# Kernel optimization log

Measured on AMD Instinct MI355X. Metric: run time of the kernel, lower is better.

## Reference

```python
import jax, jax.numpy as jnp
import numpy as np

B = 256        # trees per batch
DEPTH = 10     # complete binary tree depth -> 2^10 - 1 = 1023 internal nodes
N = 2**DEPTH - 1
IN = 128       # input_size
H = 128        # hidden_size
C = 5          # num_classes


def setup_inputs() -> dict:
    key = jax.random.key(0)
    ks = jax.random.split(key, 13)
    gdim = IN + 2 * H  # concat(x, h_left, h_right)
    inp = {"x": jax.random.normal(ks[0], (B, N, IN), jnp.float32)}
    names = ["i", "fl", "fr", "o", "u"]
    for j, nm in enumerate(names):
        inp[f"W_{nm}"] = 0.05 * jax.random.normal(ks[1 + 2 * j], (H, gdim), jnp.float32)
        inp[f"b_{nm}"] = 0.05 * jax.random.normal(ks[2 + 2 * j], (H,), jnp.float32)
    inp["W_cls"] = 0.05 * jax.random.normal(ks[11], (C, H), jnp.float32)
    inp["b_cls"] = 0.05 * jax.random.normal(ks[12], (C,), jnp.float32)
    return inp


def reference(x, W_i, b_i, W_fl, b_fl, W_fr, b_fr, W_o, b_o, W_u, b_u, W_cls, b_cls):
    # Level-order complete binary tree: node k has children 2k+1, 2k+2.
    # Bottom-up sweep; below the deepest internal level all children are
    # empty nodes with h = c = 0 (matches the original base case).
    Bb = x.shape[0]
    h = jnp.zeros((Bb, 2 ** DEPTH, H), x.dtype)
    c = jnp.zeros_like(h)
    for d in range(DEPTH - 1, -1, -1):  # fixed, small structural loop
        n = 2 ** d
        start = n - 1  # level-order offset of level d
        xs = x[:, start:start + n]            # [B, n, IN]
        hl, hr = h[:, 0::2], h[:, 1::2]       # children of node j are 2j, 2j+1 (level-local)
        cl, cr = c[:, 0::2], c[:, 1::2]
        comb = jnp.concatenate([xs, hl, hr], axis=-1)  # [B, n, IN+2H]
        lin = lambda W, b: jnp.einsum('bng,og->bno', comb, W) + b
        i = jax.nn.sigmoid(lin(W_i, b_i))
        fl = jax.nn.sigmoid(lin(W_fl, b_fl))
        fr = jax.nn.sigmoid(lin(W_fr, b_fr))
        o = jax.nn.sigmoid(lin(W_o, b_o))
        u = jnp.tanh(lin(W_u, b_u))
        c = i * u + fl * cl + fr * cr
        h = o * jnp.tanh(c)
    root_h = h[:, 0]                          # [B, H]
    logits = root_h @ W_cls.T + b_cls         # [B, C]
    return logits
```

## Files before the change

kernel.cpp:

```cpp
#include <hip/hip_runtime.h>
#include <hip/hip_bf16.h>
#include <stdint.h>


#define BATCH 256
#define NTOT 1023
#define HDIM 128
#define NCLS 5
#define GDIM 384

typedef __bf16 bf16x8 __attribute__((ext_vector_type(8)));
typedef float f32x4 __attribute__((ext_vector_type(4)));

__device__ __forceinline__ float sigmoid_f(float v) { return 1.f / (1.f + __expf(-v)); }
__device__ __forceinline__ float tanh_f(float v) { return 1.f - 2.f / (1.f + __expf(2.f * v)); }

__device__ __forceinline__ void load_lds16(const void* g, void* l) {
  __builtin_amdgcn_global_load_lds((const __attribute__((address_space(1))) unsigned int*)g,
                                   (__attribute__((address_space(3))) unsigned int*)l, 16, 0, 0);
}

__global__ __launch_bounds__(256) void pack_w(
    const float* __restrict__ W0, const float* __restrict__ W1, const float* __restrict__ W2,
    const float* __restrict__ W3, const float* __restrict__ W4, __bf16* __restrict__ PW)
{
  int t = blockIdx.x * 256 + threadIdx.x;
  int lane = t & 63;
  int chunk = t >> 6;
  int ks = chunk % 12;
  int jf = (chunk / 12) & 7;
  int g = chunk / 96;
  const float* W = (g == 0) ? W0 : (g == 1) ? W1 : (g == 2) ? W2 : (g == 3) ? W3 : W4;
  const float* s = W + (size_t)(jf * 16 + (lane & 15)) * GDIM + ks * 32 + (lane >> 4) * 8;
  float4 v0 = *(const float4*)s;
  float4 v1 = *(const float4*)(s + 4);
  bf16x8 w;
  w[0] = (__bf16)v0.x; w[1] = (__bf16)v0.y; w[2] = (__bf16)v0.z; w[3] = (__bf16)v0.w;
  w[4] = (__bf16)v1.x; w[5] = (__bf16)v1.y; w[6] = (__bf16)v1.z; w[7] = (__bf16)v1.w;
  *(bf16x8*)(PW + (size_t)t * 8) = w;
}

__constant__ int GM_LEAF[3] = {0, 3, 4};

template<bool LEAF>
__device__ __forceinline__ void tile_body(
    const float* __restrict__ x, const __bf16* __restrict__ PW,
    const __bf16* __restrict__ h_prev, const float* __restrict__ c_prev,
    __bf16* __restrict__ h_out, float* __restrict__ c_out,
    const float* __restrict__ bv0, const float* __restrict__ bv1,
    const float* __restrict__ bv2, const float* __restrict__ bv3,
    const float* __restrict__ bv4,
    int d, int m0, int j0, unsigned char* lds)
{
  const int tid = threadIdx.x;
  const int w = tid >> 6;
  const int l = tid & 63;
  const int l15 = l & 15;
  const int quad = l >> 4;
  const int q8 = quad * 8;
  const int n = 1 << d;
  const int jfb = j0 >> 4;
  constexpr int NACC = LEAF ? 3 : 5;
  constexpr int NCH = 4 * NACC;
  constexpr int BUFS = NCH * 1024;
  constexpr int NKT = LEAF ? 4 : 12;
  constexpr int NQ = NCH / 4;

  const int ms = m0 + w * 16 + l15;
  const int bs = ms >> d;
  const int ids = ms & (n - 1);
  const float* xr = x + ((size_t)bs * NTOT + (n - 1) + ids) * HDIM + q8;
  const __bf16* hr = LEAF ? (const __bf16*)nullptr
                          : h_prev + ((size_t)bs * 2 * n + 2 * ids) * HDIM + q8;

  auto stageB = [&](int t, int wks) {
    unsigned char* Bb = lds + (t & 1) * BUFS;
#pragma unroll
    for (int q = 0; q < NQ; ++q) {
      int c = w + q * 4;
      int ai = c >> 2, jfl = c & 3;
      int g = LEAF ? GM_LEAF[ai] : ai;
      const __bf16* src = PW + (((size_t)(g * 8 + jfb + jfl) * 12 + wks) * 64 + l) * 8;
      load_lds16(src, Bb + c * 1024);
    }
  };

  stageB(0, LEAF ? 0 : 4);

  bf16x8 xf[4];
#pragma unroll
  for (int kx = 0; kx < 4; ++kx) {
    float4 v0 = *(const float4*)(xr + kx * 32);
    float4 v1 = *(const float4*)(xr + kx * 32 + 4);
    bf16x8 t;
    t[0] = (__bf16)v0.x; t[1] = (__bf16)v0.y; t[2] = (__bf16)v0.z; t[3] = (__bf16)v0.w;
    t[4] = (__bf16)v1.x; t[5] = (__bf16)v1.y; t[6] = (__bf16)v1.z; t[7] = (__bf16)v1.w;
    xf[kx] = t;
  }

  bf16x8 ah[2];
  if constexpr (!LEAF) ah[0] = *(const bf16x8*)(hr);

  f32x4 acc[4][NACC];
#pragma unroll
  for (int jfl = 0; jfl < 4; ++jfl)
#pragma unroll
    for (int ai = 0; ai < NACC; ++ai)
      acc[jfl][ai] = (f32x4){0.f, 0.f, 0.f, 0.f};

#pragma unroll
  for (int t = 0; t < NKT; ++t) {
    __syncthreads();
    if (t + 1 < NKT) {
      stageB(t + 1, LEAF ? (t + 1) : ((t + 5) % 12));
      if constexpr (!LEAF) {
        if (t + 1 < 8) {
          const int o = ((t + 1) < 4) ? 0 : 1;
          ah[(t + 1) & 1] = *(const bf16x8*)(hr + o * HDIM + ((t + 1) & 3) * 32);
        }
      }
    }
    bf16x8 a;
    if constexpr (LEAF) a = xf[t];
    else a = (t < 8) ? ah[t & 1] : xf[t - 8];
    const unsigned char* Bb = lds + (t & 1) * BUFS;
#pragma unroll
    for (int ai = 0; ai < NACC; ++ai) {
#pragma unroll
      for (int jfl = 0; jfl < 4; ++jfl) {
        bf16x8 bb = *(const bf16x8*)(Bb + (ai * 4 + jfl) * 1024 + l * 16);
        acc[jfl][ai] = __builtin_amdgcn_mfma_f32_16x16x32_bf16(a, bb, acc[jfl][ai], 0, 0, 0);
      }
    }
  }

#pragma unroll
  for (int jfl = 0; jfl < 4; ++jfl) {
    const int je = j0 + jfl * 16 + l15;
    const float b0 = bv0[je], b3 = bv3[je], b4 = bv4[je];
#pragma unroll
    for (int r = 0; r < 4; ++r) {
      const int me = m0 + w * 16 + quad * 4 + r;
      const int b = me >> d;
      const int id = me & (n - 1);
      float gi = sigmoid_f(acc[jfl][0][r] + b0);
      float go = sigmoid_f(acc[jfl][LEAF ? 1 : 3][r] + b3);
      float gu = tanh_f(acc[jfl][LEAF ? 2 : 4][r] + b4);
      float cv = gi * gu;
      if constexpr (!LEAF) {
        float gl = sigmoid_f(acc[jfl][1][r] + bv1[je]);
        float gr = sigmoid_f(acc[jfl][2][r] + bv2[je]);
        size_t cbase = ((size_t)b * 2 * n + 2 * id) * HDIM + je;
        cv += gl * c_prev[cbase] + gr * c_prev[cbase + HDIM];
      }
      size_t ob = ((size_t)b * n + id) * HDIM + je;
      c_out[ob] = cv;
      h_out[ob] = (__bf16)(go * tanh_f(cv));
    }
  }
}

template<bool LEAF>
__global__ __launch_bounds__(256, (LEAF ? 5 : 4)) void level_kernel(
    const float* __restrict__ x, const __bf16* __restrict__ PW,
    const float* __restrict__ bv0, const float* __restrict__ bv1,
    const float* __restrict__ bv2, const float* __restrict__ bv3,
    const float* __restrict__ bv4,
    const __bf16* __restrict__ h_prev, const float* __restrict__ c_prev,
    __bf16* __restrict__ h_out, float* __restrict__ c_out, int d)
{
  __shared__ unsigned char lds[LEAF ? 24576 : 40960];
  tile_body<LEAF>(x, PW, h_prev, c_prev, h_out, c_out,
                  bv0, bv1, bv2, bv3, bv4, d,
                  (int)blockIdx.x * 64, (int)blockIdx.y * 64, lds);
}

#define TB_P  81920
#define TB_Q  132096
#define CSTR  132

__global__ __launch_bounds__(256, 1) void tail_kernel(
    const float* __restrict__ x, const __bf16* __restrict__ PW,
    const float* __restrict__ bv0, const float* __restrict__ bv1,
    const float* __restrict__ bv2, const float* __restrict__ bv3,
    const float* __restrict__ bv4,
    const float* __restrict__ Wcls, const float* __restrict__ bcls,
    const __bf16* __restrict__ h6, const float* __restrict__ c6,
    float* __restrict__ out)
{
  __shared__ unsigned char lds[157184];
  const int b = blockIdx.x;
  const int tid = threadIdx.x;
  const int w = tid >> 6;
  const int l = tid & 63;
  const int l15 = l & 15;
  const int quad = l >> 4;
  const int q8 = quad * 8;

  unsigned char* Ph = lds + TB_P;
  float* Pc = (float*)(lds + TB_P + 16384);
  unsigned char* Qh = lds + TB_Q;
  float* Qc = (float*)(lds + TB_Q + 8192);

  {
    const __bf16* hs = h6 + (size_t)b * 64 * HDIM;
#pragma unroll
    for (int it = 0; it < 4; ++it) {
      int idx = it * 256 + tid;
      int node = idx >> 4, i8 = idx & 15;
      bf16x8 v = *(const bf16x8*)(hs + node * HDIM + i8 * 8);
      *(bf16x8*)(Ph + node * 256 + ((i8 * 16) ^ ((node & 7) << 4))) = v;
    }
    const float* cs = c6 + (size_t)b * 64 * HDIM;
#pragma unroll
    for (int it = 0; it < 8; ++it) {
      int idx = it * 256 + tid;
      int node = idx >> 5, seg = idx & 31;
      float4 v = *(const float4*)(cs + node * HDIM + seg * 4);
      *(float4*)(Pc + node * CSTR + seg * 4) = v;
    }
  }

  for (int d = 5; d >= 0; --d) {
    const int s = 5 - d;
    const int n = 1 << d;
    const int nmf = (d == 5) ? 2 : 1;
    unsigned char* prev_h = (s & 1) ? Qh : Ph;
    float*         prev_c = (s & 1) ? Qc : Pc;
    unsigned char* cur_h  = (s & 1) ? Ph : Qh;
    float*         cur_c  = (s & 1) ? Pc : Qc;

    bf16x8 xf[2][4];
#pragma unroll
    for (int mf = 0; mf < 2; ++mf) {
      const float* xr = x + ((size_t)b * NTOT + (n - 1) + mf * 16 + l15) * HDIM + q8;
#pragma unroll
      for (int ks = 0; ks < 4; ++ks) {
        float4 v0 = *(const float4*)(xr + ks * 32);
        float4 v1 = *(const float4*)(xr + ks * 32 + 4);
        bf16x8 t;
        t[0] = (__bf16)v0.x; t[1] = (__bf16)v0.y; t[2] = (__bf16)v0.z; t[3] = (__bf16)v0.w;
        t[4] = (__bf16)v1.x; t[5] = (__bf16)v1.y; t[6] = (__bf16)v1.z; t[7] = (__bf16)v1.w;
        xf[mf][ks] = t;
      }
    }

    auto stageB = [&](int ks) {
      unsigned char* Bb = lds + (ks & 1) * 40960;
#pragma unroll
      for (int q = 0; q < 10; ++q) {
        int c = w * 10 + q;
        const __bf16* src = PW + ((size_t)(c * 12 + ks) * 64 + l) * 8;
        load_lds16(src, Bb + c * 1024);
      }
    };

    f32x4 acc[2][2][5];
#pragma unroll
    for (int mf = 0; mf < 2; ++mf)
#pragma unroll
      for (int jfl = 0; jfl < 2; ++jfl)
#pragma unroll
        for (int g = 0; g < 5; ++g)
          acc[mf][jfl][g] = (f32x4){0.f, 0.f, 0.f, 0.f};

    stageB(0);
    for (int ks = 0; ks < 12; ++ks) {
      __syncthreads();
      if (ks < 11) stageB(ks + 1);
      const unsigned char* Bb = lds + (ks & 1) * 40960;
      bf16x8 a0, a1;
      if (ks < 4) {
        a0 = xf[0][ks];
        a1 = xf[1][ks];
      } else {
        const int o = (ks < 8) ? 0 : 1;
        const int col2 = (((ks - (o ? 8 : 4)) * 32) + q8) * 2;
        int n0 = 2 * l15 + o;
        int n1 = 2 * (16 + l15) + o;
        a0 = *(const bf16x8*)(prev_h + n0 * 256 + (col2 ^ ((n0 & 7) << 4)));
        a1 = *(const bf16x8*)(prev_h + n1 * 256 + (col2 ^ ((n1 & 7) << 4)));
      }
#pragma unroll
      for (int g = 0; g < 5; ++g) {
#pragma unroll
        for (int jfl = 0; jfl < 2; ++jfl) {
          bf16x8 bb = *(const bf16x8*)(Bb + (g * 8 + w * 2 + jfl) * 1024 + l * 16);
          acc[0][jfl][g] = __builtin_amdgcn_mfma_f32_16x16x32_bf16(a0, bb, acc[0][jfl][g], 0, 0, 0);
          if (nmf == 2)
            acc[1][jfl][g] = __builtin_amdgcn_mfma_f32_16x16x32_bf16(a1, bb, acc[1][jfl][g], 0, 0, 0);
        }
      }
    }

#pragma unroll
    for (int jfl = 0; jfl < 2; ++jfl) {
      const int je = w * 32 + jfl * 16 + l15;
      const float b0 = bv0[je], b1 = bv1[je], b2 = bv2[je], b3 = bv3[je], b4 = bv4[je];
#pragma unroll
      for (int mf = 0; mf < 2; ++mf) {
#pragma unroll
        for (int r = 0; r < 4; ++r) {
          const int me = mf * 16 + quad * 4 + r;
          if (me < n) {
            float gi = sigmoid_f(acc[mf][jfl][0][r] + b0);
            float gl = sigmoid_f(acc[mf][jfl][1][r] + b1);
            float gr = sigmoid_f(acc[mf][jfl][2][r] + b2);
            float go = sigmoid_f(acc[mf][jfl][3][r] + b3);
            float gu = tanh_f(acc[mf][jfl][4][r] + b4);
            float cv = gi * gu + gl * prev_c[(2 * me) * CSTR + je]
                               + gr * prev_c[(2 * me + 1) * CSTR + je];
            cur_c[me * CSTR + je] = cv;
            *(__bf16*)(cur_h + me * 256 + ((je * 2) ^ ((me & 7) << 4))) =
                (__bf16)(go * tanh_f(cv));
          }
        }
      }
    }
  }

  __syncthreads();
  if (tid < NCLS) {
    float sacc = bcls[tid];
    for (int k = 0; k < HDIM; ++k)
      sacc += (float)(*(const __bf16*)(Ph + k * 2)) * Wcls[tid * HDIM + k];
    out[(size_t)b * NCLS + tid] = sacc;
  }
}

extern "C" void kernel_launch(void* const* d_in, const int* in_sizes, int n_in,
                              void* d_out, int out_size, void* d_ws, size_t ws_size,
                              hipStream_t stream) {
  const float* x  = (const float*)d_in[0];
  const float* W[5]  = {(const float*)d_in[1], (const float*)d_in[3], (const float*)d_in[5],
                        (const float*)d_in[7], (const float*)d_in[9]};
  const float* bv[5] = {(const float*)d_in[2], (const float*)d_in[4], (const float*)d_in[6],
                        (const float*)d_in[8], (const float*)d_in[10]};
  const float* Wcls = (const float*)d_in[11];
  const float* bcls = (const float*)d_in[12];

  uint8_t* ws = (uint8_t*)d_ws;
  __bf16* hb0 = (__bf16*)ws;
  __bf16* hb1 = (__bf16*)(ws + 33554432);
  float*  cb0 = (float*)(ws + 50331648);
  float*  cb1 = (float*)(ws + 117440512);
  __bf16* PW  = (__bf16*)(ws + 150994944);

  pack_w<<<120, 256, 0, stream>>>(W[0], W[1], W[2], W[3], W[4], PW);

  level_kernel<true><<<dim3(2048, 2), 256, 0, stream>>>(
      x, PW, bv[0], bv[1], bv[2], bv[3], bv[4], hb1, cb1, hb0, cb0, 9);
  for (int d = 8; d >= 6; --d) {
    const int p = 9 - d;
    __bf16* h_out = (p & 1) ? hb1 : hb0;
    float*  c_out = (p & 1) ? cb1 : cb0;
    const __bf16* h_prev = (p & 1) ? hb0 : hb1;
    const float*  c_prev = (p & 1) ? cb0 : cb1;
    dim3 grid((BATCH << d) >> 6, 2);
    level_kernel<false><<<grid, 256, 0, stream>>>(
        x, PW, bv[0], bv[1], bv[2], bv[3], bv[4], h_prev, c_prev, h_out, c_out, d);
  }
  tail_kernel<<<BATCH, 256, 0, stream>>>(
      x, PW, bv[0], bv[1], bv[2], bv[3], bv[4],
      Wcls, bcls, hb1, cb1, (float*)d_out);
}
```

Before: 499.7 us.

## Fuse levels 9 through 6 into one subtree kernel keeping h/c in LDS

Replaces the four per-level kernel launches for depths 9..6 with a single kernel where each 512-thread block processes a 64-leaf subtree of one tree through four levels. Intermediate h (bf16, XOR-swizzled) and c stay in LDS, so they no longer round-trip through global memory between levels, and each block now computes all 128 hidden columns against the full weight set. In exchange there is one block per CU with 157 KB of LDS, shrinking M-tiles at upper levels (down to 8 valid rows), and weights re-streamed per block.

```diff
diff --git a/kernel.cpp b/kernel.cpp
--- a/kernel.cpp
+++ b/kernel.cpp
@@ -40,17 +40,22 @@
   *(bf16x8*)(PW + (size_t)t * 8) = w;
 }
 
-__constant__ int GM_LEAF[3] = {0, 3, 4};
-
-template<bool LEAF>
-__device__ __forceinline__ void tile_body(
-    const float* __restrict__ x, const __bf16* __restrict__ PW,
-    const __bf16* __restrict__ h_prev, const float* __restrict__ c_prev,
-    __bf16* __restrict__ h_out, float* __restrict__ c_out,
+#define TB_P  81920
+#define TB_Q  132096
+#define CSTR  132
+
+template<int NMF, bool LEAF, bool LAST>
+__device__ __forceinline__ void fused_level(
+    const float* __restrict__ xp,
+    const __bf16* __restrict__ PW,
     const float* __restrict__ bv0, const float* __restrict__ bv1,
     const float* __restrict__ bv2, const float* __restrict__ bv3,
     const float* __restrict__ bv4,
-    int d, int m0, int j0, unsigned char* lds)
+    unsigned char* lds,
+    const unsigned char* prev_h, const float* prev_c,
+    unsigned char* cur_h, float* cur_c,
+    __bf16* __restrict__ gh, float* __restrict__ gc,
+    int nvalid)
 {
   const int tid = threadIdx.x;
   const int w = tid >> 6;
@@ -58,126 +63,129 @@
   const int l15 = l & 15;
   const int quad = l >> 4;
   const int q8 = quad * 8;
-  const int n = 1 << d;
-  const int jfb = j0 >> 4;
   constexpr int NACC = LEAF ? 3 : 5;
-  constexpr int NCH = 4 * NACC;
-  constexpr int BUFS = NCH * 1024;
   constexpr int NKT = LEAF ? 4 : 12;
-  constexpr int NQ = NCH / 4;
-
-  const int ms = m0 + w * 16 + l15;
-  const int bs = ms >> d;
-  const int ids = ms & (n - 1);
-  const float* xr = x + ((size_t)bs * NTOT + (n - 1) + ids) * HDIM + q8;
-  const __bf16* hr = LEAF ? (const __bf16*)nullptr
-                          : h_prev + ((size_t)bs * 2 * n + 2 * ids) * HDIM + q8;
-
-  auto stageB = [&](int t, int wks) {
-    unsigned char* Bb = lds + (t & 1) * BUFS;
+  constexpr int NCH = NACC * 8;
+  constexpr int NQ = NCH / 8;
+
+  auto stageB = [&](int ks) {
+    unsigned char* Bb = lds + (ks & 1) * 40960;
 #pragma unroll
     for (int q = 0; q < NQ; ++q) {
-      int c = w + q * 4;
-      int ai = c >> 2, jfl = c & 3;
-      int g = LEAF ? GM_LEAF[ai] : ai;
-      const __bf16* src = PW + (((size_t)(g * 8 + jfb + jfl) * 12 + wks) * 64 + l) * 8;
+      int c = w * NQ + q;
+      int ai = c >> 3, jf = c & 7;
+      int g = LEAF ? (ai ? ai + 2 : 0) : ai;
+      const __bf16* src = PW + (((size_t)(g * 8 + jf) * 12 + ks) * 64 + l) * 8;
       load_lds16(src, Bb + c * 1024);
     }
   };
 
-  stageB(0, LEAF ? 0 : 4);
-
-  bf16x8 xf[4];
-#pragma unroll
-  for (int kx = 0; kx < 4; ++kx) {
-    float4 v0 = *(const float4*)(xr + kx * 32);
-    float4 v1 = *(const float4*)(xr + kx * 32 + 4);
-    bf16x8 t;
-    t[0] = (__bf16)v0.x; t[1] = (__bf16)v0.y; t[2] = (__bf16)v0.z; t[3] = (__bf16)v0.w;
-    t[4] = (__bf16)v1.x; t[5] = (__bf16)v1.y; t[6] = (__bf16)v1.z; t[7] = (__bf16)v1.w;
-    xf[kx] = t;
-  }
-
-  bf16x8 ah[2];
-  if constexpr (!LEAF) ah[0] = *(const bf16x8*)(hr);
-
-  f32x4 acc[4][NACC];
-#pragma unroll
-  for (int jfl = 0; jfl < 4; ++jfl)
+  stageB(0);
+
+  bf16x8 xf[NMF][4];
+#pragma unroll
+  for (int mf = 0; mf < NMF; ++mf) {
+    const float* xr = xp + (size_t)(mf * 16 + l15) * HDIM + q8;
+#pragma unroll
+    for (int kx = 0; kx < 4; ++kx) {
+      float4 v0 = *(const float4*)(xr + kx * 32);
+      float4 v1 = *(const float4*)(xr + kx * 32 + 4);
+      bf16x8 t;
+      t[0] = (__bf16)v0.x; t[1] = (__bf16)v0.y; t[2] = (__bf16)v0.z; t[3] = (__bf16)v0.w;
+      t[4] = (__bf16)v1.x; t[5] = (__bf16)v1.y; t[6] = (__bf16)v1.z; t[7] = (__bf16)v1.w;
+      xf[mf][kx] = t;
+    }
+  }
+
+  f32x4 acc[NMF][NACC];
+#pragma unroll
+  for (int mf = 0; mf < NMF; ++mf)
 #pragma unroll
     for (int ai = 0; ai < NACC; ++ai)
-      acc[jfl][ai] = (f32x4){0.f, 0.f, 0.f, 0.f};
-
-#pragma unroll
-  for (int t = 0; t < NKT; ++t) {
+      acc[mf][ai] = (f32x4){0.f, 0.f, 0.f, 0.f};
+
+#pragma unroll
+  for (int ks = 0; ks < NKT; ++ks) {
     __syncthreads();
-    if (t + 1 < NKT) {
-      stageB(t + 1, LEAF ? (t + 1) : ((t + 5) % 12));
-      if constexpr (!LEAF) {
-        if (t + 1 < 8) {
-          const int o = ((t + 1) < 4) ? 0 : 1;
-          ah[(t + 1) & 1] = *(const bf16x8*)(hr + o * HDIM + ((t + 1) & 3) * 32);
+    if (ks + 1 < NKT) stageB(ks + 1);
+    const unsigned char* Bb = lds + (ks & 1) * 40960;
+    bf16x8 a[NMF];
+#pragma unroll
+    for (int mf = 0; mf < NMF; ++mf) {
+      if (LEAF || ks < 4) {
+        a[mf] = xf[mf][LEAF ? ks : (ks & 3)];
+      } else {
+        const int o = (ks < 8) ? 0 : 1;
+        const int col2 = ((ks - (o ? 8 : 4)) * 32 + q8) * 2;
+        const int n = 2 * (mf * 16 + l15) + o;
+        a[mf] = *(const bf16x8*)(prev_h + n * 256 + (col2 ^ ((n & 7) << 4)));
+      }
+    }
+#pragma unroll
+    for (int ai = 0; ai < NACC; ++ai) {
+      bf16x8 bb = *(const bf16x8*)(Bb + (ai * 8 + w) * 1024 + l * 16);
+#pragma unroll
+      for (int mf = 0; mf < NMF; ++mf)
+        acc[mf][ai] = __builtin_amdgcn_mfma_f32_16x16x32_bf16(a[mf], bb, acc[mf][ai], 0, 0, 0);
+    }
+  }
+
+  const int je = w * 16 + l15;
+  const float b0 = bv0[je], b3v = bv3[je], b4v = bv4[je];
+#pragma unroll
+  for (int mf = 0; mf < NMF; ++mf) {
+#pragma unroll
+    for (int r = 0; r < 4; ++r) {
+      const int me = mf * 16 + quad * 4 + r;
+      if (me < nvalid) {
+        float gi = sigmoid_f(acc[mf][0][r] + b0);
+        float go = sigmoid_f(acc[mf][LEAF ? 1 : 3][r] + b3v);
+        float gu = tanh_f(acc[mf][LEAF ? 2 : 4][r] + b4v);
+        float cv = gi * gu;
+        if constexpr (!LEAF) {
+          float gl = sigmoid_f(acc[mf][1][r] + bv1[je]);
+          float gr = sigmoid_f(acc[mf][2][r] + bv2[je]);
+          cv += gl * prev_c[(2 * me) * CSTR + je] + gr * prev_c[(2 * me + 1) * CSTR + je];
         }
-      }
-    }
-    bf16x8 a;
-    if constexpr (LEAF) a = xf[t];
-    else a = (t < 8) ? ah[t & 1] : xf[t - 8];
-    const unsigned char* Bb = lds + (t & 1) * BUFS;
-#pragma unroll
-    for (int ai = 0; ai < NACC; ++ai) {
-#pragma unroll
-      for (int jfl = 0; jfl < 4; ++jfl) {
-        bf16x8 bb = *(const bf16x8*)(Bb + (ai * 4 + jfl) * 1024 + l * 16);
-        acc[jfl][ai] = __builtin_amdgcn_mfma_f32_16x16x32_bf16(a, bb, acc[jfl][ai], 0, 0, 0);
-      }
-    }
-  }
-
-#pragma unroll
-  for (int jfl = 0; jfl < 4; ++jfl) {
-    const int je = j0 + jfl * 16 + l15;
-    const float b0 = bv0[je], b3 = bv3[je], b4 = bv4[je];
-#pragma unroll
-    for (int r = 0; r < 4; ++r) {
-      const int me = m0 + w * 16 + quad * 4 + r;
-      const int b = me >> d;
-      const int id = me & (n - 1);
-      float gi = sigmoid_f(acc[jfl][0][r] + b0);
-      float go = sigmoid_f(acc[jfl][LEAF ? 1 : 3][r] + b3);
-      float gu = tanh_f(acc[jfl][LEAF ? 2 : 4][r] + b4);
-      float cv = gi * gu;
-      if constexpr (!LEAF) {
-        float gl = sigmoid_f(acc[jfl][1][r] + bv1[je]);
-        float gr = sigmoid_f(acc[jfl][2][r] + bv2[je]);
-        size_t cbase = ((size_t)b * 2 * n + 2 * id) * HDIM + je;
-        cv += gl * c_prev[cbase] + gr * c_prev[cbase + HDIM];
-      }
-      size_t ob = ((size_t)b * n + id) * HDIM + je;
-      c_out[ob] = cv;
-      h_out[ob] = (__bf16)(go * tanh_f(cv));
-    }
-  }
-}
-
-template<bool LEAF>
-__global__ __launch_bounds__(256, (LEAF ? 5 : 4)) void level_kernel(
+        float hv = go * tanh_f(cv);
+        if constexpr (LAST) {
+          gc[(size_t)me * HDIM + je] = cv;
+          gh[(size_t)me * HDIM + je] = (__bf16)hv;
+        } else {
+          cur_c[me * CSTR + je] = cv;
+          *(__bf16*)(cur_h + me * 256 + ((je * 2) ^ ((me & 7) << 4))) = (__bf16)hv;
+        }
+      }
+    }
+  }
+}
+
+__global__ __launch_bounds__(512, 1) void fused_top(
     const float* __restrict__ x, const __bf16* __restrict__ PW,
     const float* __restrict__ bv0, const float* __restrict__ bv1,
     const float* __restrict__ bv2, const float* __restrict__ bv3,
     const float* __restrict__ bv4,
-    const __bf16* __restrict__ h_prev, const float* __restrict__ c_prev,
-    __bf16* __restrict__ h_out, float* __restrict__ c_out, int d)
+    __bf16* __restrict__ h6, float* __restrict__ c6)
 {
-  __shared__ unsigned char lds[LEAF ? 24576 : 40960];
-  tile_body<LEAF>(x, PW, h_prev, c_prev, h_out, c_out,
-                  bv0, bv1, bv2, bv3, bv4, d,
-                  (int)blockIdx.x * 64, (int)blockIdx.y * 64, lds);
-}
-
-#define TB_P  81920
-#define TB_Q  132096
-#define CSTR  132
+  __shared__ unsigned char lds[157184];
+  const int b = blockIdx.x >> 3;
+  const int s = blockIdx.x & 7;
+  unsigned char* Ph = lds + TB_P;
+  float* Pc = (float*)(lds + TB_P + 16384);
+  unsigned char* Qh = lds + TB_Q;
+  float* Qc = (float*)(lds + TB_Q + 8192);
+  const size_t xb = (size_t)b * NTOT;
+
+  fused_level<4, true, false>(x + (xb + 511 + s * 64) * HDIM, PW,
+      bv0, bv1, bv2, bv3, bv4, lds, nullptr, nullptr, Ph, Pc, nullptr, nullptr, 64);
+  fused_level<2, false, false>(x + (xb + 255 + s * 32) * HDIM, PW,
+      bv0, bv1, bv2, bv3, bv4, lds, Ph, Pc, Qh, Qc, nullptr, nullptr, 32);
+  fused_level<1, false, false>(x + (xb + 127 + s * 16) * HDIM, PW,
+      bv0, bv1, bv2, bv3, bv4, lds, Qh, Qc, Ph, Pc, nullptr, nullptr, 16);
+  fused_level<1, false, true>(x + (xb + 63 + s * 8) * HDIM, PW,
+      bv0, bv1, bv2, bv3, bv4, lds, Ph, Pc, nullptr, nullptr,
+      h6 + ((size_t)b * 64 + s * 8) * HDIM, c6 + ((size_t)b * 64 + s * 8) * HDIM, 8);
+}
 
 __global__ __launch_bounds__(256, 1) void tail_kernel(
     const float* __restrict__ x, const __bf16* __restrict__ PW,
@@ -340,26 +348,15 @@
   const float* bcls = (const float*)d_in[12];
 
   uint8_t* ws = (uint8_t*)d_ws;
-  __bf16* hb0 = (__bf16*)ws;
   __bf16* hb1 = (__bf16*)(ws + 33554432);
-  float*  cb0 = (float*)(ws + 50331648);
   float*  cb1 = (float*)(ws + 117440512);
   __bf16* PW  = (__bf16*)(ws + 150994944);
 
   pack_w<<<120, 256, 0, stream>>>(W[0], W[1], W[2], W[3], W[4], PW);
 
-  level_kernel<true><<<dim3(2048, 2), 256, 0, stream>>>(
-      x, PW, bv[0], bv[1], bv[2], bv[3], bv[4], hb1, cb1, hb0, cb0, 9);
-  for (int d = 8; d >= 6; --d) {
-    const int p = 9 - d;
-    __bf16* h_out = (p & 1) ? hb1 : hb0;
-    float*  c_out = (p & 1) ? cb1 : cb0;
-    const __bf16* h_prev = (p & 1) ? hb0 : hb1;
-    const float*  c_prev = (p & 1) ? cb0 : cb1;
-    dim3 grid((BATCH << d) >> 6, 2);
-    level_kernel<false><<<grid, 256, 0, stream>>>(
-        x, PW, bv[0], bv[1], bv[2], bv[3], bv[4], h_prev, c_prev, h_out, c_out, d);
-  }
+  fused_top<<<BATCH * 8, 512, 0, stream>>>(
+      x, PW, bv[0], bv[1], bv[2], bv[3], bv[4], hb1, cb1);
+
   tail_kernel<<<BATCH, 256, 0, stream>>>(
       x, PW, bv[0], bv[1], bv[2], bv[3], bv[4],
       Wcls, bcls, hb1, cb1, (float*)d_out);
```

After: 565.7 us. +13.2%, slower.
